# Performance work log

Hardware: AMD Instinct MI355X
Metric: run time of the kernel (lower is better)

## Reference

```python
import jax, jax.numpy as jnp
import numpy as np

K = 3
TAU = 1.0
EPS = 1e-8


def _route_dense(z, k, tau):
    """RouterTopK forward -> dense combine weights [N, L].
    Matches torch: topk values, softmax(topv/tau). Softmax is permutation
    invariant so sorted top_k gives identical math to sorted=False."""
    topi = jax.lax.top_k(z, k)[1]                      # [N, k] int32
    topv = jnp.take_along_axis(z, topi, axis=1)        # [N, k]
    w = jax.nn.softmax(topv / (tau + EPS), axis=1)     # [N, k]
    N, L = z.shape
    dw = jnp.zeros((N, L), z.dtype)
    dw = dw.at[jnp.arange(N)[:, None], topi].add(w)
    return dw


def _apply_mixture(x, dw, W):
    """y[n] = sum_e dw[n,e] * (W[e] @ x[n]).  Loop over the small fixed
    expert count (12); equivalent math to the sort+grouped-GEMM dispatch."""
    y = jnp.zeros((x.shape[0], W.shape[1]), x.dtype)
    for e in range(W.shape[0]):
        y = y + (x @ W[e].T) * dw[:, e:e + 1]
    return y


def setup_inputs() -> dict:
    key = jax.random.key(0)
    ks = jax.random.split(key, 8)
    B, T, D_in, H, D_out, L, d_addr = 4, 2048, 1024, 4096, 1024, 12, 64

    def unitize(U):
        U = U - U.mean(axis=1, keepdims=True)
        return U / (jnp.linalg.norm(U, axis=1, keepdims=True) + EPS)

    x = jax.random.normal(ks[0], (B, T, D_in), jnp.float32)
    P_w = jax.random.normal(ks[1], (d_addr, D_in), jnp.float32) / np.sqrt(D_in)
    U1 = unitize(jax.random.normal(ks[2], (L, d_addr), jnp.float32))
    U2 = unitize(jax.random.normal(ks[3], (L, d_addr), jnp.float32))
    U3 = unitize(jax.random.normal(ks[4], (L, d_addr), jnp.float32))
    W1 = jax.random.normal(ks[5], (L, H, D_in), jnp.float32)
    W1 = W1 / jnp.linalg.norm(W1.reshape(L, -1), axis=1)[:, None, None]
    W2 = jax.random.normal(ks[6], (L, D_out, H), jnp.float32)
    W2 = W2 / jnp.linalg.norm(W2.reshape(L, -1), axis=1)[:, None, None]
    b2 = jax.random.normal(ks[7], (L, D_out), jnp.float32)
    b2 = b2 / jnp.linalg.norm(b2, axis=1, keepdims=True)
    return {"x": x, "P_w": P_w, "U1": U1, "U2": U2, "U3": U3,
            "W1": W1, "W2": W2, "b2": b2}


def reference(x, P_w, U1, U2, U3, W1, W2, b2):
    B, T, D = x.shape
    x_flat = x.reshape(B * T, D)                       # [N, D_in]
    x_addr = x_flat @ P_w.T                            # [N, d_addr]
    dw1 = _route_dense(x_addr @ U1.T, K, TAU)          # [N, L]
    dw2 = _route_dense(x_addr @ U2.T, K, TAU)
    dw3 = _route_dense(x_addr @ U3.T, K, TAU)
    h = _apply_mixture(x_flat, dw1, W1)                # [N, H]
    h = jax.nn.gelu(h, approximate=False)              # nn.GELU (exact)
    y = _apply_mixture(h, dw2, W2)                     # [N, D_out]
    y = y + dw3 @ b2                                   # grouped bias add
    return y.reshape(B, T, -1)
```

## Files before the change

kernel.cpp:

```cpp
#include <hip/hip_runtime.h>
#include <math.h>

#define DEVI __device__ __forceinline__
typedef unsigned short u16;
typedef unsigned int u32;
typedef unsigned char u8;
typedef float f32x4 __attribute__((ext_vector_type(4)));

static constexpr int CAP = 8192;

DEVI u16 f2b(float f) {
  u32 x = __builtin_bit_cast(u32, f);
  u32 r = (x + 0x7fffu + ((x >> 16) & 1u)) >> 16;
  return (u16)r;
}
DEVI float b2f(u16 u) { return __builtin_bit_cast(float, (u32)u << 16); }

DEVI u32 f2fp8(float f) {
  u32 x = __builtin_bit_cast(u32, f);
  u32 s = (x >> 24) & 0x80u;
  u32 ax = x & 0x7fffffffu;
  if (ax >= 0x43e80000u) return s | 0x7eu;
  if (ax < 0x3a800000u) return s;
  if (ax < 0x3c800000u) {
    float m = __builtin_bit_cast(float, ax) * 512.0f;
    return s | (u32)rintf(m);
  }
  u32 r = ax + 0x7ffffu + ((ax >> 20) & 1u);
  return s | (((r >> 23) - 120u) << 3) | ((r >> 20) & 7u);
}

DEVI void async16(const void* g, void* l) {
  __builtin_amdgcn_global_load_lds((const __attribute__((address_space(1))) void*)g,
                                   (__attribute__((address_space(3))) void*)l, 16, 0, 0);
}

__global__ void cvt8_k(const float* __restrict__ s0, u8* __restrict__ d0,
                       const float* __restrict__ s1, u8* __restrict__ d1, long n) {
  long nq0 = n / 4, nq = nq0 * 2;
  long stride = (long)gridDim.x * blockDim.x;
  for (long q = (long)blockIdx.x * blockDim.x + threadIdx.x; q < nq; q += stride) {
    long qi = q; const float* s = s0; u8* d = d0;
    if (qi >= nq0) { qi -= nq0; s = s1; d = d1; }
    float4 v = ((const float4*)s)[qi];
    uchar4 o;
    o.x = (u8)f2fp8(v.x * 1024.f); o.y = (u8)f2fp8(v.y * 1024.f);
    o.z = (u8)f2fp8(v.z * 1024.f); o.w = (u8)f2fp8(v.w * 1024.f);
    ((uchar4*)d)[qi] = o;
  }
}

__global__ __launch_bounds__(256) void xrouter_k(
    const float* __restrict__ x, const float* __restrict__ Pw,
    const float* __restrict__ U1, const float* __restrict__ U2, const float* __restrict__ U3,
    const float* __restrict__ b2,
    int* __restrict__ cnt, int* __restrict__ ltok, float* __restrict__ lwgt,
    float* __restrict__ out, u8* __restrict__ xb) {
  __shared__ __align__(16) char sm[22400];
  float*  xs  = (float*)sm;
  float*  pws = (float*)(sm + 2176);
  float*  us  = (float*)(sm + 2176);
  double* xa  = (double*)(sm + 11968);
  double* zz  = (double*)(sm + 19584);
  int*    se  = (int*)(sm + 22144);
  float*  swg = (float*)(sm + 22272);

  const int tid = threadIdx.x;
  const int tok0 = blockIdx.x * 8;
  const int tok = tid >> 5, dg = tid & 31;

  double a0 = 0, a1 = 0, a2 = 0, a3 = 0;

  for (int kc = 0; kc < 16; ++kc) {
    if (tid < 128) {
      int t = tid >> 4, c4 = tid & 15;
      size_t goff = (size_t)(tok0 + t) * 1024 + kc * 64 + c4 * 4;
      float4 v = *(const float4*)&x[goff];
      *(float4*)&xs[t * 68 + c4 * 4] = v;
      uchar4 o;
      o.x = (u8)f2fp8(v.x); o.y = (u8)f2fp8(v.y);
      o.z = (u8)f2fp8(v.z); o.w = (u8)f2fp8(v.w);
      *(uchar4*)&xb[goff] = o;
    }
#pragma unroll
    for (int j = 0; j < 4; ++j) {
      int f = tid + 256 * j;
      int r = f >> 4, c4 = f & 15;
      *(float4*)&pws[r * 68 + c4 * 4] = *(const float4*)&Pw[(size_t)r * 1024 + kc * 64 + c4 * 4];
    }
    __syncthreads();
    const float* xrow = &xs[tok * 68];
    const float* p0 = &pws[dg * 68];
    const float* p1 = &pws[(dg + 32) * 68];
#pragma unroll
    for (int k4 = 0; k4 < 16; ++k4) {
      float4 xv = *(const float4*)&xrow[k4 * 4];
      float4 q0 = *(const float4*)&p0[k4 * 4];
      float4 q1 = *(const float4*)&p1[k4 * 4];
      a0 += (double)xv.x * q0.x + (double)xv.y * q0.y;
      a1 += (double)xv.z * q0.z + (double)xv.w * q0.w;
      a2 += (double)xv.x * q1.x + (double)xv.y * q1.y;
      a3 += (double)xv.z * q1.z + (double)xv.w * q1.w;
    }
    __syncthreads();
  }

  xa[tok * 66 + dg] = a0 + a1;
  xa[tok * 66 + dg + 32] = a2 + a3;
  if (tid < 144) {
#pragma unroll
    for (int j = 0; j < 4; ++j) {
      int f = tid * 4 + j;
      int r = f >> 4, c4 = f & 15;
      const float* U = (r < 12) ? (U1 + r * 64) : (r < 24 ? U2 + (r - 12) * 64 : U3 + (r - 24) * 64);
      *(float4*)&us[r * 68 + c4 * 4] = *(const float4*)&U[c4 * 4];
    }
  }
  __syncthreads();

#pragma unroll
  for (int rep = 0; rep < 2; ++rep) {
    int idx = tid + 256 * rep;
    int tk = idx >> 6, re = idx & 63;
    if (re < 36) {
      double acc = 0;
      const double* xr = &xa[tk * 66];
      const float* ur = &us[re * 68];
      for (int k = 0; k < 64; ++k) acc += xr[k] * (double)ur[k];
      zz[tk * 40 + re] = acc;
    }
  }
  __syncthreads();

  if (tid < 24) {
    const int tk = tid & 7, r = tid >> 3;
    const double* z = &zz[tk * 40 + r * 12];
    double v0 = -1e300, v1 = -1e300, v2 = -1e300;
    int i0 = 0, i1 = 0, i2 = 0;
    for (int e = 0; e < 12; ++e) {
      double v = z[e];
      if (v > v0)      { v2 = v1; i2 = i1; v1 = v0; i1 = i0; v0 = v; i0 = e; }
      else if (v > v1) { v2 = v1; i2 = i1; v1 = v; i1 = e; }
      else if (v > v2) { v2 = v; i2 = e; }
    }
    const double inv_tau = 1.0 / (1.0 + 1e-8);
    double e1 = exp((v1 - v0) * inv_tau), e2 = exp((v2 - v0) * inv_tau);
    double s = 1.0 / (1.0 + e1 + e2);
    double w0 = s, w1 = e1 * s, w2 = e2 * s;
    int n = tok0 + tk;
    if (r < 2) {
      int jj3[3] = { i0, i1, i2 };
      double ww[3] = { w0, w1, w2 };
      for (int j = 0; j < 3; ++j) {
        int slot = (r * 3 + j) * 12 + jj3[j];
        int pos = atomicAdd(&cnt[slot], 1);
        ltok[slot * CAP + pos] = n;
        lwgt[slot * CAP + pos] = (float)ww[j];
      }
    } else {
      se[tk * 4 + 0] = i0; se[tk * 4 + 1] = i1; se[tk * 4 + 2] = i2;
      swg[tk * 4 + 0] = (float)w0; swg[tk * 4 + 1] = (float)w1; swg[tk * 4 + 2] = (float)w2;
    }
  }
  __syncthreads();

#pragma unroll
  for (int j = 0; j < 8; ++j) {
    int f = tid + 256 * j;
    int tk = f >> 8, c4 = f & 255;
    const float w0 = swg[tk * 4 + 0], w1 = swg[tk * 4 + 1], w2 = swg[tk * 4 + 2];
    float4 a = *(const float4*)&b2[(size_t)se[tk * 4 + 0] * 1024 + c4 * 4];
    float4 b = *(const float4*)&b2[(size_t)se[tk * 4 + 1] * 1024 + c4 * 4];
    float4 d = *(const float4*)&b2[(size_t)se[tk * 4 + 2] * 1024 + c4 * 4];
    float4 o;
    o.x = w0 * a.x + w1 * b.x + w2 * d.x;
    o.y = w0 * a.y + w1 * b.y + w2 * d.y;
    o.z = w0 * a.z + w1 * b.z + w2 * d.z;
    o.w = w0 * a.w + w1 * b.w + w2 * d.w;
    *(float4*)&out[(size_t)(tok0 + tk) * 1024 + c4 * 4] = o;
  }
}

__global__ void build_k(const int* __restrict__ cnt, int2* __restrict__ desc,
                        int* __restrict__ ntl) {
  int t = threadIdx.x;
  if (t < 6) {
    int nt = 0;
    for (int e = 0; e < 12; ++e) {
      int c = cnt[t * 12 + e];
      for (int s = 0; s < c; s += 128) { desc[t * 96 + nt] = make_int2(e, s); ++nt; }
    }
    ntl[t] = nt;
  }
}

template<int KB, int NOUT, bool ADD, typename CT>
__global__ __launch_bounds__(256, 4) void moe_gemm(
    const u8* __restrict__ A, const u8* __restrict__ W, CT* __restrict__ C,
    float outScale,
    const int* __restrict__ cnt12, const int* __restrict__ ltok12,
    const float* __restrict__ lwgt12,
    const int2* __restrict__ desc, const int* __restrict__ ntl) {
  unsigned lin = blockIdx.y * gridDim.x + blockIdx.x;
  unsigned q = (gridDim.x * gridDim.y) >> 3;
  unsigned swz = (lin & 7) * q + (lin >> 3);
  int tile = swz % gridDim.x;
  int ntile = swz / gridDim.x;
  if (tile >= *ntl) return;
  const int2 dd = desc[tile];
  const int e = dd.x, rowStart = dd.y;
  const int rows = min(128, cnt12[e] - rowStart);
  const int base = e * CAP + rowStart;

  __shared__ __align__(16) u8 As[2][8192];
  __shared__ __align__(16) u8 Bs[2][8192];
  __shared__ int tokL[128];
  __shared__ float wgtL[128];

  const int tid = threadIdx.x;
  const int lane = tid & 63, w = tid >> 6;
  if (tid < 128) {
    int li = min(tid, rows - 1);
    tokL[tid] = ltok12[base + li];
    wgtL[tid] = lwgt12[base + li];
  }
  __syncthreads();

  const int srcSwz = (((tid & 3) ^ ((tid >> 3) & 3)) * 16);
  const u8* aSrc[2]; const u8* bSrc[2];
#pragma unroll
  for (int i = 0; i < 2; ++i) {
    int r = i * 64 + (tid >> 2);
    aSrc[i] = A + (size_t)tokL[min(r, rows - 1)] * KB + srcSwz;
    bSrc[i] = W + ((size_t)e * NOUT + ntile * 128 + r) * KB + srcSwz;
  }

  f32x4 acc[4][4] = {};
  const int wr = w >> 1, wc = w & 1;
  const int sxr = (lane >> 1) & 3;
  const int p8 = ((lane >> 4) & 1) * 8;
  const int roff0 = 16 * (((lane >> 5) | 0) ^ sxr) + p8;
  const int roff1 = 16 * (((lane >> 5) | 2) ^ sxr) + p8;
  constexpr int NT = KB / 64;

#define STAGE(kt_) do { int ko_ = (kt_) * 64; int b_ = (kt_) & 1;               \
    async16(aSrc[0] + ko_, &As[b_][tid * 16]);                                  \
    async16(aSrc[1] + ko_, &As[b_][(256 + tid) * 16]);                          \
    async16(bSrc[0] + ko_, &Bs[b_][tid * 16]);                                  \
    async16(bSrc[1] + ko_, &Bs[b_][(256 + tid) * 16]); } while (0)

  STAGE(0);
  __syncthreads();
  for (int kt = 0; kt < NT; ++kt) {
    if (kt + 1 < NT) STAGE(kt + 1);
    const u8* Ab = &As[kt & 1][0];
    const u8* Bb = &Bs[kt & 1][0];
#pragma unroll
    for (int kk = 0; kk < 2; ++kk) {
      const int ro = kk ? roff1 : roff0;
      long bf[4];
#pragma unroll
      for (int ni = 0; ni < 4; ++ni) {
        int rB = wc * 64 + ni * 16 + (lane & 15);
        bf[ni] = *(const long*)&Bb[rB * 64 + ro];
      }
#pragma unroll
      for (int mi = 0; mi < 4; ++mi) {
        int rA = wr * 64 + mi * 16 + (lane & 15);
        long af = *(const long*)&Ab[rA * 64 + ro];
#pragma unroll
        for (int ni = 0; ni < 4; ++ni)
          acc[mi][ni] = __builtin_amdgcn_mfma_f32_16x16x32_fp8_fp8(af, bf[ni], acc[mi][ni], 0, 0, 0);
      }
    }
    __syncthreads();
  }
#undef STAGE

#pragma unroll
  for (int mi = 0; mi < 4; ++mi) {
    int lr0 = wr * 64 + mi * 16 + ((lane >> 4) << 2);
#pragma unroll
    for (int rr = 0; rr < 4; ++rr) {
      int lrow = lr0 + rr;
      bool rowok = lrow < rows;
      int tok = tokL[lrow];
      float wv = wgtL[lrow] * outScale;
      if constexpr (sizeof(CT) == 2) {
        u32* cp32 = (u32*)((u16*)C + (size_t)tok * NOUT + ntile * 128 + wc * 64 + (lane & 14));
#pragma unroll
        for (int ni = 0; ni < 4; ++ni) {
          float v = acc[mi][ni][rr] * wv;
          float vo = __shfl_xor(v, 1);
          if (rowok && !(lane & 1)) {
            float lo = v, hi = vo;
            if (ADD) {
              u32 curv = cp32[ni * 8];
              lo += b2f((u16)(curv & 0xffffu));
              hi += b2f((u16)(curv >> 16));
            }
            cp32[ni * 8] = (u32)f2b(lo) | ((u32)f2b(hi) << 16);
          }
        }
      } else {
        if (rowok) {
          float* cp = (float*)C + (size_t)tok * NOUT + ntile * 128 + wc * 64 + (lane & 15);
#pragma unroll
          for (int ni = 0; ni < 4; ++ni) {
            float val = acc[mi][ni][rr] * wv;
            float* p = cp + ni * 16;
            *p = ADD ? (*p + val) : val;
          }
        }
      }
    }
  }
}

DEVI float gelu1(float v) { return 0.5f * v * (1.0f + erff(v * 0.70710678118654752f)); }
__global__ void gelu8_k(const u32* __restrict__ h, uint2* __restrict__ h8, long n8) {
  long stride = (long)gridDim.x * blockDim.x;
  const uint4* hp = (const uint4*)h;
  for (long i = (long)blockIdx.x * blockDim.x + threadIdx.x; i < n8; i += stride) {
    uint4 v = hp[i];
    u32 words[4] = { v.x, v.y, v.z, v.w };
    u32 lo = 0, hi = 0;
#pragma unroll
    for (int j = 0; j < 4; ++j) {
      float f0 = b2f((u16)(words[j] & 0xffffu));
      float f1 = b2f((u16)(words[j] >> 16));
      u32 c0 = f2fp8(gelu1(f0) * 256.f);
      u32 c1 = f2fp8(gelu1(f1) * 256.f);
      u32 pair = c0 | (c1 << 8);
      if (j < 2) lo |= pair << (16 * j);
      else       hi |= pair << (16 * (j - 2));
    }
    h8[i] = make_uint2(lo, hi);
  }
}

extern "C" void kernel_launch(void* const* d_in, const int* in_sizes, int n_in,
                              void* d_out, int out_size, void* d_ws, size_t ws_size,
                              hipStream_t stream) {
  const float* x  = (const float*)d_in[0];
  const float* Pw = (const float*)d_in[1];
  const float* U1 = (const float*)d_in[2];
  const float* U2 = (const float*)d_in[3];
  const float* U3 = (const float*)d_in[4];
  const float* W1 = (const float*)d_in[5];
  const float* W2 = (const float*)d_in[6];
  const float* b2 = (const float*)d_in[7];
  float* out = (float*)d_out;

  char* ws = (char*)d_ws;
  size_t o = 0;
  u8*  W1b = (u8*)(ws + o); o += (size_t)12 * 4096 * 1024;
  u8*  W2b = (u8*)(ws + o); o += (size_t)12 * 1024 * 4096;
  u8*  xb  = (u8*)(ws + o); o += (size_t)8192 * 1024;
  u16* h   = (u16*)(ws + o); o += (size_t)8192 * 4096 * 2;
  u8*  h8  = (u8*)(ws + o); o += (size_t)8192 * 4096;
  int* cnt = (int*)(ws + o); o += 512;
  int2* desc = (int2*)(ws + o); o += (size_t)6 * 96 * sizeof(int2);
  o = (o + 255) & ~(size_t)255;
  int* ntl = (int*)(ws + o); o += 256;
  int* ltok = (int*)(ws + o); o += (size_t)6 * 12 * CAP * 4;
  float* lwgt = (float*)(ws + o); o += (size_t)6 * 12 * CAP * 4;
  if (ws_size < o) return;

  hipMemsetAsync(cnt, 0, 512, stream);
  cvt8_k<<<4096, 256, 0, stream>>>(W1, W1b, W2, W2b, (long)12 * 4096 * 1024);
  xrouter_k<<<1024, 256, 0, stream>>>(x, Pw, U1, U2, U3, b2, cnt, ltok, lwgt, out, xb);
  build_k<<<1, 64, 0, stream>>>(cnt, desc, ntl);

  const float s1 = 1.0f / 1024.f;
  const float s2 = 1.0f / (1024.f * 256.f);

  {
    dim3 g(80, 32);
    int s;
    s = 0; moe_gemm<1024, 4096, false, u16><<<g, 256, 0, stream>>>(xb, W1b, h, s1, cnt + s * 12, ltok + (size_t)s * 12 * CAP, lwgt + (size_t)s * 12 * CAP, desc + s * 96, ntl + s);
    s = 1; moe_gemm<1024, 4096, true , u16><<<g, 256, 0, stream>>>(xb, W1b, h, s1, cnt + s * 12, ltok + (size_t)s * 12 * CAP, lwgt + (size_t)s * 12 * CAP, desc + s * 96, ntl + s);
    s = 2; moe_gemm<1024, 4096, true , u16><<<g, 256, 0, stream>>>(xb, W1b, h, s1, cnt + s * 12, ltok + (size_t)s * 12 * CAP, lwgt + (size_t)s * 12 * CAP, desc + s * 96, ntl + s);
  }

  gelu8_k<<<2048, 256, 0, stream>>>((const u32*)h, (uint2*)h8, (long)8192 * 4096 / 8);

  {
    dim3 g(80, 8);
    int s;
    s = 3; moe_gemm<4096, 1024, true, float><<<g, 256, 0, stream>>>(h8, W2b, out, s2, cnt + s * 12, ltok + (size_t)s * 12 * CAP, lwgt + (size_t)s * 12 * CAP, desc + s * 96, ntl + s);
    s = 4; moe_gemm<4096, 1024, true, float><<<g, 256, 0, stream>>>(h8, W2b, out, s2, cnt + s * 12, ltok + (size_t)s * 12 * CAP, lwgt + (size_t)s * 12 * CAP, desc + s * 96, ntl + s);
    s = 5; moe_gemm<4096, 1024, true, float><<<g, 256, 0, stream>>>(h8, W2b, out, s2, cnt + s * 12, ltok + (size_t)s * 12 * CAP, lwgt + (size_t)s * 12 * CAP, desc + s * 96, ntl + s);
  }
}
```

Baseline: 856.7 us.

## Double-buffer router projection and process 16 tokens per block

The router kernel now handles 16 tokens per block instead of 8, so each P_w chunk loaded into shared memory is reused across twice as many tokens and total P_w traffic is halved. Global loads for the next chunk are prefetched into registers and written into a double-buffered shared tile, removing one barrier per iteration. The P_w tile in shared memory is also stored with a rotating column swizzle to avoid bank conflicts. In exchange, shared memory per block rises to about 57 KB and only 512 blocks are launched, which may lower occupancy and parallelism.

```diff
diff --git a/kernel.cpp b/kernel.cpp
--- a/kernel.cpp
+++ b/kernel.cpp
@@ -56,57 +56,83 @@
     const float* __restrict__ b2,
     int* __restrict__ cnt, int* __restrict__ ltok, float* __restrict__ lwgt,
     float* __restrict__ out, u8* __restrict__ xb) {
-  __shared__ __align__(16) char sm[22400];
-  float*  xs  = (float*)sm;
-  float*  pws = (float*)(sm + 2176);
-  float*  us  = (float*)(sm + 2176);
-  double* xa  = (double*)(sm + 11968);
-  double* zz  = (double*)(sm + 19584);
-  int*    se  = (int*)(sm + 22144);
-  float*  swg = (float*)(sm + 22272);
+  __shared__ __align__(16) char sm[57600];
+  float*  pws = (float*)sm;
+  float*  xs  = (float*)(sm + 34816);
+  double* xa  = (double*)(sm + 43520);
+  double* zz  = (double*)(sm + 51968);
+  int*    se  = (int*)(sm + 57088);
+  float*  swg = (float*)(sm + 57344);
+  float*  us  = (float*)sm;
 
   const int tid = threadIdx.x;
-  const int tok0 = blockIdx.x * 8;
-  const int tok = tid >> 5, dg = tid & 31;
-
-  double a0 = 0, a1 = 0, a2 = 0, a3 = 0;
-
+  const int tok0 = blockIdx.x * 16;
+  const int sr = tid >> 4, sc = tid & 15;
+
+  float4 rpw[4]; float4 rxv;
+
+  auto LOADC = [&](int kc) {
+    size_t xoff = (size_t)(tok0 + sr) * 1024 + kc * 64 + sc * 4;
+    rxv = *(const float4*)&x[xoff];
+    uchar4 o8;
+    o8.x = (u8)f2fp8(rxv.x); o8.y = (u8)f2fp8(rxv.y);
+    o8.z = (u8)f2fp8(rxv.z); o8.w = (u8)f2fp8(rxv.w);
+    *(uchar4*)&xb[xoff] = o8;
+#pragma unroll
+    for (int j = 0; j < 4; ++j) {
+      int f = tid + 256 * j; int pr = f >> 4, pc = f & 15;
+      rpw[j] = *(const float4*)&Pw[(size_t)pr * 1024 + kc * 64 + pc * 4];
+    }
+  };
+  auto WRITEC = [&](int b) {
+    float* xbuf = xs + b * 1088;
+    float* pbuf = pws + b * 4352;
+    *(float4*)&xbuf[sr * 68 + sc * 4] = rxv;
+#pragma unroll
+    for (int j = 0; j < 4; ++j) {
+      int f = tid + 256 * j; int pr = f >> 4, pc = f & 15;
+      int pos = (pc + pr + (pr >> 3)) & 15;
+      *(float4*)&pbuf[pr * 68 + pos * 4] = rpw[j];
+    }
+  };
+
+  const int dg = tid & 31, tg = tid >> 5;
+  const int rot0 = (dg + (dg >> 3)) & 15;
+  const int rot1 = (rot0 + 4) & 15;
+  double a00l = 0, a00h = 0, a01l = 0, a01h = 0;
+  double a10l = 0, a10h = 0, a11l = 0, a11h = 0;
+
+  LOADC(0);
   for (int kc = 0; kc < 16; ++kc) {
-    if (tid < 128) {
-      int t = tid >> 4, c4 = tid & 15;
-      size_t goff = (size_t)(tok0 + t) * 1024 + kc * 64 + c4 * 4;
-      float4 v = *(const float4*)&x[goff];
-      *(float4*)&xs[t * 68 + c4 * 4] = v;
-      uchar4 o;
-      o.x = (u8)f2fp8(v.x); o.y = (u8)f2fp8(v.y);
-      o.z = (u8)f2fp8(v.z); o.w = (u8)f2fp8(v.w);
-      *(uchar4*)&xb[goff] = o;
-    }
-#pragma unroll
-    for (int j = 0; j < 4; ++j) {
-      int f = tid + 256 * j;
-      int r = f >> 4, c4 = f & 15;
-      *(float4*)&pws[r * 68 + c4 * 4] = *(const float4*)&Pw[(size_t)r * 1024 + kc * 64 + c4 * 4];
-    }
+    int b = kc & 1;
+    WRITEC(b);
     __syncthreads();
-    const float* xrow = &xs[tok * 68];
-    const float* p0 = &pws[dg * 68];
-    const float* p1 = &pws[(dg + 32) * 68];
+    if (kc < 15) LOADC(kc + 1);
+    const float* xbuf = xs + b * 1088;
+    const float* pbuf = pws + b * 4352;
 #pragma unroll
     for (int k4 = 0; k4 < 16; ++k4) {
-      float4 xv = *(const float4*)&xrow[k4 * 4];
-      float4 q0 = *(const float4*)&p0[k4 * 4];
-      float4 q1 = *(const float4*)&p1[k4 * 4];
-      a0 += (double)xv.x * q0.x + (double)xv.y * q0.y;
-      a1 += (double)xv.z * q0.z + (double)xv.w * q0.w;
-      a2 += (double)xv.x * q1.x + (double)xv.y * q1.y;
-      a3 += (double)xv.z * q1.z + (double)xv.w * q1.w;
-    }
-    __syncthreads();
-  }
-
-  xa[tok * 66 + dg] = a0 + a1;
-  xa[tok * 66 + dg + 32] = a2 + a3;
+      float4 xv0 = *(const float4*)&xbuf[tg * 68 + k4 * 4];
+      float4 xv1 = *(const float4*)&xbuf[(tg + 8) * 68 + k4 * 4];
+      float4 q0 = *(const float4*)&pbuf[dg * 68 + ((k4 + rot0) & 15) * 4];
+      float4 q1 = *(const float4*)&pbuf[(dg + 32) * 68 + ((k4 + rot1) & 15) * 4];
+      a00l += (double)xv0.x * q0.x + (double)xv0.y * q0.y;
+      a00h += (double)xv0.z * q0.z + (double)xv0.w * q0.w;
+      a01l += (double)xv0.x * q1.x + (double)xv0.y * q1.y;
+      a01h += (double)xv0.z * q1.z + (double)xv0.w * q1.w;
+      a10l += (double)xv1.x * q0.x + (double)xv1.y * q0.y;
+      a10h += (double)xv1.z * q0.z + (double)xv1.w * q0.w;
+      a11l += (double)xv1.x * q1.x + (double)xv1.y * q1.y;
+      a11h += (double)xv1.z * q1.z + (double)xv1.w * q1.w;
+    }
+  }
+
+  xa[tg * 66 + dg]        = a00l + a00h;
+  xa[tg * 66 + dg + 32]   = a01l + a01h;
+  xa[(tg + 8) * 66 + dg]      = a10l + a10h;
+  xa[(tg + 8) * 66 + dg + 32] = a11l + a11h;
+  __syncthreads();
+
   if (tid < 144) {
 #pragma unroll
     for (int j = 0; j < 4; ++j) {
@@ -119,10 +145,10 @@
   __syncthreads();
 
 #pragma unroll
-  for (int rep = 0; rep < 2; ++rep) {
+  for (int rep = 0; rep < 3; ++rep) {
     int idx = tid + 256 * rep;
-    int tk = idx >> 6, re = idx & 63;
-    if (re < 36) {
+    if (idx < 576) {
+      int tk = idx / 36, re = idx - tk * 36;
       double acc = 0;
       const double* xr = &xa[tk * 66];
       const float* ur = &us[re * 68];
@@ -132,8 +158,8 @@
   }
   __syncthreads();
 
-  if (tid < 24) {
-    const int tk = tid & 7, r = tid >> 3;
+  if (tid < 48) {
+    const int tk = tid & 15, r = tid >> 4;
     const double* z = &zz[tk * 40 + r * 12];
     double v0 = -1e300, v1 = -1e300, v2 = -1e300;
     int i0 = 0, i1 = 0, i2 = 0;
@@ -165,7 +191,7 @@
   __syncthreads();
 
 #pragma unroll
-  for (int j = 0; j < 8; ++j) {
+  for (int j = 0; j < 16; ++j) {
     int f = tid + 256 * j;
     int tk = f >> 8, c4 = f & 255;
     const float w0 = swg[tk * 4 + 0], w1 = swg[tk * 4 + 1], w2 = swg[tk * 4 + 2];
@@ -369,7 +395,7 @@
 
   hipMemsetAsync(cnt, 0, 512, stream);
   cvt8_k<<<4096, 256, 0, stream>>>(W1, W1b, W2, W2b, (long)12 * 4096 * 1024);
-  xrouter_k<<<1024, 256, 0, stream>>>(x, Pw, U1, U2, U3, b2, cnt, ltok, lwgt, out, xb);
+  xrouter_k<<<512, 256, 0, stream>>>(x, Pw, U1, U2, U3, b2, cnt, ltok, lwgt, out, xb);
   build_k<<<1, 64, 0, stream>>>(cnt, desc, ntl);
 
   const float s1 = 1.0f / 1024.f;
```

Result: slower. 942.7 us (+10.0%).

## Split fused router into address-projection and routing kernels, move x fp8 cast

Applied to the files above, without the earlier changes.

The fused x-router kernel is split in two. One kernel computes the 64-dim address projection with one thread per (token, dim) output, reading x and P_w straight from global memory, and writes the result to a double buffer in workspace. A second kernel does top-k routing and the bias add over 16 tokens per block. The fp8 conversion of x moves into the weight conversion kernel. The goal is more parallelism and less serialized shared-memory staging in the router, at the cost of an extra launch, a global round trip for the projection, and uncached redundant reads of P_w.

```diff
diff --git a/kernel.cpp b/kernel.cpp
--- a/kernel.cpp
+++ b/kernel.cpp
@@ -36,105 +36,91 @@
 }
 
 __global__ void cvt8_k(const float* __restrict__ s0, u8* __restrict__ d0,
-                       const float* __restrict__ s1, u8* __restrict__ d1, long n) {
-  long nq0 = n / 4, nq = nq0 * 2;
+                       const float* __restrict__ s1, u8* __restrict__ d1, long n,
+                       const float* __restrict__ s2, u8* __restrict__ d2, long n2) {
+  long nq0 = n / 4, nq2 = n2 / 4, nq = nq0 * 2 + nq2;
   long stride = (long)gridDim.x * blockDim.x;
   for (long q = (long)blockIdx.x * blockDim.x + threadIdx.x; q < nq; q += stride) {
-    long qi = q; const float* s = s0; u8* d = d0;
-    if (qi >= nq0) { qi -= nq0; s = s1; d = d1; }
+    long qi = q; const float* s; u8* d; float sc = 1024.f;
+    if (qi < nq0) { s = s0; d = d0; }
+    else if (qi < 2 * nq0) { qi -= nq0; s = s1; d = d1; }
+    else { qi -= 2 * nq0; s = s2; d = d2; sc = 1.0f; }
     float4 v = ((const float4*)s)[qi];
     uchar4 o;
-    o.x = (u8)f2fp8(v.x * 1024.f); o.y = (u8)f2fp8(v.y * 1024.f);
-    o.z = (u8)f2fp8(v.z * 1024.f); o.w = (u8)f2fp8(v.w * 1024.f);
+    o.x = (u8)f2fp8(v.x * sc); o.y = (u8)f2fp8(v.y * sc);
+    o.z = (u8)f2fp8(v.z * sc); o.w = (u8)f2fp8(v.w * sc);
     ((uchar4*)d)[qi] = o;
   }
 }
 
-__global__ __launch_bounds__(256) void xrouter_k(
+__global__ __launch_bounds__(256) void xaddr_k(
     const float* __restrict__ x, const float* __restrict__ Pw,
+    double* __restrict__ xa_g) {
+  const int tid = threadIdx.x;
+  const int tok = blockIdx.x * 16 + (tid >> 4);
+  const int d = blockIdx.y * 16 + (tid & 15);
+  const float* xr = x + (size_t)tok * 1024;
+  const float* pr = Pw + (size_t)d * 1024;
+  double al = 0, ah = 0;
+#pragma unroll 8
+  for (int k4 = 0; k4 < 256; ++k4) {
+    float4 xv = *(const float4*)&xr[k4 * 4];
+    float4 pv = *(const float4*)&pr[k4 * 4];
+    al += (double)xv.x * pv.x + (double)xv.y * pv.y;
+    ah += (double)xv.z * pv.z + (double)xv.w * pv.w;
+  }
+  xa_g[(size_t)tok * 64 + d] = al + ah;
+}
+
+__global__ __launch_bounds__(256) void route2_k(
+    const double* __restrict__ xa_g,
     const float* __restrict__ U1, const float* __restrict__ U2, const float* __restrict__ U3,
     const float* __restrict__ b2,
     int* __restrict__ cnt, int* __restrict__ ltok, float* __restrict__ lwgt,
-    float* __restrict__ out, u8* __restrict__ xb) {
-  __shared__ __align__(16) char sm[22400];
-  float*  xs  = (float*)sm;
-  float*  pws = (float*)(sm + 2176);
-  float*  us  = (float*)(sm + 2176);
-  double* xa  = (double*)(sm + 11968);
-  double* zz  = (double*)(sm + 19584);
-  int*    se  = (int*)(sm + 22144);
-  float*  swg = (float*)(sm + 22272);
+    float* __restrict__ out) {
+  __shared__ double xa[16][66];
+  __shared__ float us[36][68];
+  __shared__ double zz[16][40];
+  __shared__ int se[16][4];
+  __shared__ float swg[16][4];
 
   const int tid = threadIdx.x;
-  const int tok0 = blockIdx.x * 8;
-  const int tok = tid >> 5, dg = tid & 31;
-
-  double a0 = 0, a1 = 0, a2 = 0, a3 = 0;
-
-  for (int kc = 0; kc < 16; ++kc) {
-    if (tid < 128) {
-      int t = tid >> 4, c4 = tid & 15;
-      size_t goff = (size_t)(tok0 + t) * 1024 + kc * 64 + c4 * 4;
-      float4 v = *(const float4*)&x[goff];
-      *(float4*)&xs[t * 68 + c4 * 4] = v;
-      uchar4 o;
-      o.x = (u8)f2fp8(v.x); o.y = (u8)f2fp8(v.y);
-      o.z = (u8)f2fp8(v.z); o.w = (u8)f2fp8(v.w);
-      *(uchar4*)&xb[goff] = o;
-    }
-#pragma unroll
-    for (int j = 0; j < 4; ++j) {
-      int f = tid + 256 * j;
-      int r = f >> 4, c4 = f & 15;
-      *(float4*)&pws[r * 68 + c4 * 4] = *(const float4*)&Pw[(size_t)r * 1024 + kc * 64 + c4 * 4];
-    }
-    __syncthreads();
-    const float* xrow = &xs[tok * 68];
-    const float* p0 = &pws[dg * 68];
-    const float* p1 = &pws[(dg + 32) * 68];
-#pragma unroll
-    for (int k4 = 0; k4 < 16; ++k4) {
-      float4 xv = *(const float4*)&xrow[k4 * 4];
-      float4 q0 = *(const float4*)&p0[k4 * 4];
-      float4 q1 = *(const float4*)&p1[k4 * 4];
-      a0 += (double)xv.x * q0.x + (double)xv.y * q0.y;
-      a1 += (double)xv.z * q0.z + (double)xv.w * q0.w;
-      a2 += (double)xv.x * q1.x + (double)xv.y * q1.y;
-      a3 += (double)xv.z * q1.z + (double)xv.w * q1.w;
-    }
-    __syncthreads();
-  }
-
-  xa[tok * 66 + dg] = a0 + a1;
-  xa[tok * 66 + dg + 32] = a2 + a3;
+  const int tok0 = blockIdx.x * 16;
+
+  {
+    const int tk = tid >> 4, j = tid & 15;
+    const double* src = &xa_g[(size_t)(tok0 + tk) * 64 + j * 4];
+#pragma unroll
+    for (int m = 0; m < 4; ++m) xa[tk][j * 4 + m] = src[m];
+  }
   if (tid < 144) {
 #pragma unroll
     for (int j = 0; j < 4; ++j) {
       int f = tid * 4 + j;
       int r = f >> 4, c4 = f & 15;
       const float* U = (r < 12) ? (U1 + r * 64) : (r < 24 ? U2 + (r - 12) * 64 : U3 + (r - 24) * 64);
-      *(float4*)&us[r * 68 + c4 * 4] = *(const float4*)&U[c4 * 4];
-    }
-  }
-  __syncthreads();
-
-#pragma unroll
-  for (int rep = 0; rep < 2; ++rep) {
+      *(float4*)&us[r][c4 * 4] = *(const float4*)&U[c4 * 4];
+    }
+  }
+  __syncthreads();
+
+#pragma unroll
+  for (int rep = 0; rep < 3; ++rep) {
     int idx = tid + 256 * rep;
-    int tk = idx >> 6, re = idx & 63;
-    if (re < 36) {
+    if (idx < 576) {
+      int tk = idx / 36, re = idx - tk * 36;
       double acc = 0;
-      const double* xr = &xa[tk * 66];
-      const float* ur = &us[re * 68];
+      const double* xr = &xa[tk][0];
+      const float* ur = &us[re][0];
       for (int k = 0; k < 64; ++k) acc += xr[k] * (double)ur[k];
-      zz[tk * 40 + re] = acc;
-    }
-  }
-  __syncthreads();
-
-  if (tid < 24) {
-    const int tk = tid & 7, r = tid >> 3;
-    const double* z = &zz[tk * 40 + r * 12];
+      zz[tk][re] = acc;
+    }
+  }
+  __syncthreads();
+
+  if (tid < 48) {
+    const int tk = tid & 15, r = tid >> 4;
+    const double* z = &zz[tk][r * 12];
     double v0 = -1e300, v1 = -1e300, v2 = -1e300;
     int i0 = 0, i1 = 0, i2 = 0;
     for (int e = 0; e < 12; ++e) {
@@ -158,20 +144,20 @@
         lwgt[slot * CAP + pos] = (float)ww[j];
       }
     } else {
-      se[tk * 4 + 0] = i0; se[tk * 4 + 1] = i1; se[tk * 4 + 2] = i2;
-      swg[tk * 4 + 0] = (float)w0; swg[tk * 4 + 1] = (float)w1; swg[tk * 4 + 2] = (float)w2;
-    }
-  }
-  __syncthreads();
-
-#pragma unroll
-  for (int j = 0; j < 8; ++j) {
+      se[tk][0] = i0; se[tk][1] = i1; se[tk][2] = i2;
+      swg[tk][0] = (float)w0; swg[tk][1] = (float)w1; swg[tk][2] = (float)w2;
+    }
+  }
+  __syncthreads();
+
+#pragma unroll
+  for (int j = 0; j < 16; ++j) {
     int f = tid + 256 * j;
     int tk = f >> 8, c4 = f & 255;
-    const float w0 = swg[tk * 4 + 0], w1 = swg[tk * 4 + 1], w2 = swg[tk * 4 + 2];
-    float4 a = *(const float4*)&b2[(size_t)se[tk * 4 + 0] * 1024 + c4 * 4];
-    float4 b = *(const float4*)&b2[(size_t)se[tk * 4 + 1] * 1024 + c4 * 4];
-    float4 d = *(const float4*)&b2[(size_t)se[tk * 4 + 2] * 1024 + c4 * 4];
+    const float w0 = swg[tk][0], w1 = swg[tk][1], w2 = swg[tk][2];
+    float4 a = *(const float4*)&b2[(size_t)se[tk][0] * 1024 + c4 * 4];
+    float4 b = *(const float4*)&b2[(size_t)se[tk][1] * 1024 + c4 * 4];
+    float4 d = *(const float4*)&b2[(size_t)se[tk][2] * 1024 + c4 * 4];
     float4 o;
     o.x = w0 * a.x + w1 * b.x + w2 * d.x;
     o.y = w0 * a.y + w1 * b.y + w2 * d.y;
@@ -359,6 +345,7 @@
   u8*  xb  = (u8*)(ws + o); o += (size_t)8192 * 1024;
   u16* h   = (u16*)(ws + o); o += (size_t)8192 * 4096 * 2;
   u8*  h8  = (u8*)(ws + o); o += (size_t)8192 * 4096;
+  double* xa_g = (double*)(ws + o); o += (size_t)8192 * 64 * 8;
   int* cnt = (int*)(ws + o); o += 512;
   int2* desc = (int2*)(ws + o); o += (size_t)6 * 96 * sizeof(int2);
   o = (o + 255) & ~(size_t)255;
@@ -368,8 +355,10 @@
   if (ws_size < o) return;
 
   hipMemsetAsync(cnt, 0, 512, stream);
-  cvt8_k<<<4096, 256, 0, stream>>>(W1, W1b, W2, W2b, (long)12 * 4096 * 1024);
-  xrouter_k<<<1024, 256, 0, stream>>>(x, Pw, U1, U2, U3, b2, cnt, ltok, lwgt, out, xb);
+  cvt8_k<<<4096, 256, 0, stream>>>(W1, W1b, W2, W2b, (long)12 * 4096 * 1024,
+                                   x, xb, (long)8192 * 1024);
+  xaddr_k<<<dim3(512, 4), 256, 0, stream>>>(x, Pw, xa_g);
+  route2_k<<<512, 256, 0, stream>>>(xa_g, U1, U2, U3, b2, cnt, ltok, lwgt, out);
   build_k<<<1, 64, 0, stream>>>(cnt, desc, ntl);
 
   const float s1 = 1.0f / 1024.f;
```

After: 1.100 ms. 1.28x slower.
